# Kernel tuning notes

Measured on AMD Instinct MI355X. Metric: run time of the kernel, lower is better.

The kernel has to match this reference:

```python
import jax, jax.numpy as jnp
import numpy as np
from jax import lax

FPLANE = 64
T = 8          # num_segments
HEADS = 4
EPS = 1e-5


def _conv2d(x, w, b):
    # x: [N,C,H,W], w: [O,I,kh,kw]
    y = lax.conv_general_dilated(x, w, (1, 1), 'SAME',
                                 dimension_numbers=('NCHW', 'OIHW', 'NCHW'))
    return y + b[None, :, None, None]


def _conv3d_grouped(x, w, b, groups):
    # x: [N,C,D,H,W], w: [O, C//groups, kd,kh,kw]
    y = lax.conv_general_dilated(x, w, (1, 1, 1), 'SAME',
                                 dimension_numbers=('NCDHW', 'OIDHW', 'NCDHW'),
                                 feature_group_count=groups)
    return y + b[None, :, None, None, None]


def setup_inputs() -> dict:
    key = jax.random.key(0)
    ks = jax.random.split(key, 5)
    N, C, H, W = T * 16, FPLANE, 56, 56
    x = jax.random.normal(ks[0], (N, C, H, W), dtype=jnp.float32)
    attn_w = jax.random.normal(ks[1], (HEADS, C, 3, 3), dtype=jnp.float32) * 0.05
    attn_b = jax.random.normal(ks[2], (HEADS,), dtype=jnp.float32) * 0.05
    bn_gamma = jnp.ones((C,), dtype=jnp.float32)
    bn_beta = jnp.zeros((C,), dtype=jnp.float32)
    conv3d_w = jax.random.normal(ks[3], (2, C // 2, 3, 3, 3), dtype=jnp.float32) * 0.05
    conv3d_b = jax.random.normal(ks[4], (2,), dtype=jnp.float32) * 0.05
    return {'x': x, 'attn_w': attn_w, 'attn_b': attn_b,
            'bn_gamma': bn_gamma, 'bn_beta': bn_beta,
            'conv3d_w': conv3d_w, 'conv3d_b': conv3d_b}


def reference(x, attn_w, attn_b, bn_gamma, bn_beta, conv3d_w, conv3d_b):
    N, C, H, W = x.shape
    B = N // T
    half = C // 2
    quarter = C // 4

    # spatial attention: conv2d -> ReLU -> Sigmoid, per-head gating
    attn = jax.nn.sigmoid(jax.nn.relu(_conv2d(x, attn_w, attn_b)))  # [N,HEADS,H,W]
    xh = x.reshape(N, HEADS, C // HEADS, H, W) * attn[:, :, None]
    x2 = xh.reshape(N, C, H, W)

    # [B*T,C,H,W] -> [B,C,T,H,W]
    x5 = x2.reshape(B, T, C, H, W).transpose(0, 2, 1, 3, 4)

    # BatchNorm3d (training-mode batch statistics) + ReLU
    mean = jnp.mean(x5, axis=(0, 2, 3, 4), keepdims=True)
    var = jnp.var(x5, axis=(0, 2, 3, 4), keepdims=True)
    x_bn = (x5 - mean) * lax.rsqrt(var + EPS)
    x_bn = x_bn * bn_gamma[None, :, None, None, None] + bn_beta[None, :, None, None, None]
    x_bn_relu = jax.nn.relu(x_bn)

    # grouped conv3d gate (2 groups, 1 output channel each), tanh
    gate = jnp.tanh(_conv3d_grouped(x_bn_relu, conv3d_w, conv3d_b, groups=2))  # [B,2,T,H,W]
    g1 = gate[:, 0:1]
    g2 = gate[:, 1:2]

    x_g1 = x5[:, :half]
    x_g2 = x5[:, half:]
    y1 = g1 * x_g1
    y2 = g2 * x_g2
    r1 = x_g1 - y1
    r2 = x_g2 - y2

    pad_t = ((0, 0), (0, 0), (0, 1), (0, 0), (0, 0))
    pad_b = ((0, 0), (0, 0), (1, 0), (0, 0), (0, 0))
    y1 = jnp.pad(y1[:, :, 1:], pad_t) + r1   # left shift in time, zero pad
    y2 = jnp.pad(y2[:, :, :-1], pad_b) + r2  # right shift in time, zero pad

    # interleave sub-halves: view [B,2,C/4,T,H,W] -> permute -> [B,C/2,T,H,W]
    def interleave(y):
        return (y.reshape(B, 2, quarter, T, H, W)
                 .transpose(0, 2, 1, 3, 4, 5)
                 .reshape(B, half, T, H, W))

    y = jnp.concatenate([interleave(y1), interleave(y2)], axis=1)  # [B,C,T,H,W]
    return y.transpose(0, 2, 1, 3, 4).reshape(N, C, H, W)
```

## Files before the change

kernel.cpp:

```cpp
#include <hip/hip_runtime.h>
#include <hip/hip_bf16.h>

#define HW 3136
#define CTOT 64
#define NTOT 128
#define BB 16
#define TTT 8

static __device__ __forceinline__ float bf2f(unsigned short u) {
    union { unsigned int ui; float f; } v;
    v.ui = ((unsigned int)u) << 16;
    return v.f;
}
static __device__ __forceinline__ unsigned short f2bf(float f) {
    union { float f; unsigned int u; } v;
    v.f = f;
    unsigned int u = v.u;
    unsigned int r = (u + 0x7fffu + ((u >> 16) & 1u)) >> 16;
    return (unsigned short)r;
}

__global__ void k_repack(const float* __restrict__ aw, float* __restrict__ wpk) {
    const int idx = blockIdx.x * 256 + threadIdx.x;
    if (idx >= 2304) return;
    const int hd = idx & 3;
    const int kw = (idx >> 2) % 3;
    const int dh = (idx / 12) % 3;
    const int c = idx / 36;
    wpk[idx] = aw[hd * 576 + c * 9 + dh * 3 + kw];
}

__global__ __launch_bounds__(128) void k_attn(const float* __restrict__ x,
                                              const float* __restrict__ wpk,
                                              const float* __restrict__ ab,
                                              float* __restrict__ attn,
                                              float* __restrict__ stats) {
    const int tile = blockIdx.x % 49;
    const int n = blockIdx.x / 49;
    const int chunk = threadIdx.x >> 4;
    const int qi = threadIdx.x & 15;
    const int quad = tile * 16 + qi;
    const int q = quad % 14;
    const int h = quad / 14;
    const int w0 = q * 4;

    __shared__ float wl[2304];
    __shared__ float l[8][16][17];
    __shared__ float4 abuf[4][16];

    const float* xn = x + (size_t)n * CTOT * HW;
    const int c0 = chunk * 8;

    auto loadrows = [&](int c, float r[3][6]) {
#pragma unroll
        for (int dh = 0; dh < 3; ++dh) {
            const int hh = h + dh - 1;
            const bool v = (hh >= 0) && (hh < 56);
            const float* row = xn + c * HW + (v ? hh : h) * 56 + w0;
            const float m = v ? 1.f : 0.f;
            const float4 mid = *(const float4*)row;
            const float e0 = row[(q > 0) ? -1 : 0] * ((q > 0) ? m : 0.f);
            const float e5 = row[(q < 13) ? 4 : 3] * ((q < 13) ? m : 0.f);
            r[dh][0] = e0;
            r[dh][1] = mid.x * m; r[dh][2] = mid.y * m;
            r[dh][3] = mid.z * m; r[dh][4] = mid.w * m;
            r[dh][5] = e5;
        }
    };

    float bufA[3][6], bufB[3][6];
    loadrows(c0, bufA);

#pragma unroll
    for (int i = 0; i < 18; ++i) wl[threadIdx.x + i * 128] = wpk[threadIdx.x + i * 128];
    __syncthreads();

    float acc[4][4];
#pragma unroll
    for (int hd = 0; hd < 4; ++hd)
#pragma unroll
        for (int j = 0; j < 4; ++j) acc[hd][j] = 0.f;

    float midst[8][4];

#pragma unroll
    for (int i = 0; i < 8; ++i) {
        float (*cur)[6] = (i & 1) ? bufB : bufA;
        float (*nxt)[6] = (i & 1) ? bufA : bufB;
        if (i < 7) loadrows(c0 + i + 1, nxt);

        midst[i][0] = cur[1][1]; midst[i][1] = cur[1][2];
        midst[i][2] = cur[1][3]; midst[i][3] = cur[1][4];

        const int c = c0 + i;
#pragma unroll
        for (int dh = 0; dh < 3; ++dh) {
            const float* wb = &wl[c * 36 + dh * 12];
            const float4 wk0 = *(const float4*)(wb);
            const float4 wk1 = *(const float4*)(wb + 4);
            const float4 wk2 = *(const float4*)(wb + 8);
#pragma unroll
            for (int j = 0; j < 4; ++j) {
                const float a0 = cur[dh][j], a1 = cur[dh][j + 1], a2 = cur[dh][j + 2];
                acc[0][j] = fmaf(a0, wk0.x, fmaf(a1, wk1.x, fmaf(a2, wk2.x, acc[0][j])));
                acc[1][j] = fmaf(a0, wk0.y, fmaf(a1, wk1.y, fmaf(a2, wk2.y, acc[1][j])));
                acc[2][j] = fmaf(a0, wk0.z, fmaf(a1, wk1.z, fmaf(a2, wk2.z, acc[2][j])));
                acc[3][j] = fmaf(a0, wk0.w, fmaf(a1, wk1.w, fmaf(a2, wk2.w, acc[3][j])));
            }
        }
    }

    float* mine = &l[chunk][qi][0];
#pragma unroll
    for (int hd = 0; hd < 4; ++hd)
#pragma unroll
        for (int j = 0; j < 4; ++j) mine[hd * 4 + j] = acc[hd][j];
    __syncthreads();

    if (threadIdx.x < 64) {
        const int hd = threadIdx.x >> 4;
        const int rq = threadIdx.x & 15;
        float s0 = ab[hd], s1 = s0, s2 = s0, s3 = s0;
#pragma unroll
        for (int cch = 0; cch < 8; ++cch) {
            const float* p = &l[cch][rq][hd * 4];
            s0 += p[0]; s1 += p[1]; s2 += p[2]; s3 += p[3];
        }
        float4 o;
        o.x = s0 > 0.f ? 1.f / (1.f + __expf(-s0)) : 0.5f;
        o.y = s1 > 0.f ? 1.f / (1.f + __expf(-s1)) : 0.5f;
        o.z = s2 > 0.f ? 1.f / (1.f + __expf(-s2)) : 0.5f;
        o.w = s3 > 0.f ? 1.f / (1.f + __expf(-s3)) : 0.5f;
        *(float4*)(attn + (size_t)(n * 4 + hd) * HW + (tile * 16 + rq) * 4) = o;
        abuf[hd][rq] = o;
    }
    __syncthreads();

    const int head = chunk >> 1;
    const float4 a4 = abuf[head][qi];
    float s[8], sq[8];
#pragma unroll
    for (int i = 0; i < 8; ++i) {
        const float v0 = midst[i][0] * a4.x;
        const float v1 = midst[i][1] * a4.y;
        const float v2 = midst[i][2] * a4.z;
        const float v3 = midst[i][3] * a4.w;
        s[i] = v0 + v1 + v2 + v3;
        sq[i] = v0 * v0 + v1 * v1 + v2 * v2 + v3 * v3;
    }
#pragma unroll
    for (int i = 0; i < 8; ++i) { mine[i] = s[i]; mine[8 + i] = sq[i]; }
    __syncthreads();
    {
        const int ch2 = threadIdx.x >> 4;
        const int k = threadIdx.x & 15;
        float t = 0.f;
#pragma unroll
        for (int qq = 0; qq < 16; ++qq) t += l[ch2][qq][k];
        const int cc = ch2 * 8 + (k & 7);
        const int rep = blockIdx.x & 15;
        atomicAdd(&stats[rep * 128 + (k >> 3) * 64 + cc], t);
    }
}

__global__ void k_finalize(const float* __restrict__ stats,
                           const float* __restrict__ gamma,
                           const float* __restrict__ beta,
                           float* __restrict__ ss) {
    const int c = threadIdx.x;
    float S = 0.f, Q = 0.f;
#pragma unroll
    for (int r = 0; r < 16; ++r) {
        S += stats[r * 128 + c];
        Q += stats[r * 128 + 64 + c];
    }
    const float cnt = 401408.0f;
    const float mean = S / cnt;
    const float var = Q / cnt - mean * mean;
    const float scale = gamma[c] * rsqrtf(var + 1e-5f);
    ss[c] = scale;
    ss[64 + c] = beta[c] - mean * scale;
}

__global__ __launch_bounds__(256) void k_xbnr(const float* __restrict__ x,
                                              const float* __restrict__ attn,
                                              const float* __restrict__ ss,
                                              unsigned short* __restrict__ xbnr) {
    const int i4 = blockIdx.x * 256 + threadIdx.x;
    const int base = i4 * 4;
    const int plane = base / HW;
    const int i = base - plane * HW;
    const int c = plane & 63;
    const int n = plane >> 6;
    const float4 xv = *(const float4*)(x + (size_t)base);
    const float4 av = *(const float4*)(attn + (size_t)(n * 4 + (c >> 4)) * HW + i);
    const float sc = ss[c], sh = ss[64 + c];
    ushort4 o;
    o.x = f2bf(fmaxf(fmaf(xv.x * av.x, sc, sh), 0.f));
    o.y = f2bf(fmaxf(fmaf(xv.y * av.y, sc, sh), 0.f));
    o.z = f2bf(fmaxf(fmaf(xv.z * av.z, sc, sh), 0.f));
    o.w = f2bf(fmaxf(fmaf(xv.w * av.w, sc, sh), 0.f));
    *(ushort4*)(xbnr + (size_t)base) = o;
}

__global__ __launch_bounds__(128) void k_conv3d(const unsigned short* __restrict__ xbnr,
                                                const float* __restrict__ w3,
                                                const float* __restrict__ b3,
                                                float* __restrict__ gate) {
    const int tile = blockIdx.x % 49;
    const int oc = (blockIdx.x / 49) & 1;
    const int b = blockIdx.x / 98;
    const int chunk = threadIdx.x >> 4;
    const int qi = threadIdx.x & 15;
    const int quad = tile * 16 + qi;
    const int q = quad % 14;
    const int h = quad / 14;
    const int w0 = q * 4;

    float acc[8][4];
#pragma unroll
    for (int t = 0; t < 8; ++t)
#pragma unroll
        for (int j = 0; j < 4; ++j) acc[t][j] = 0.f;

    const int ic0 = chunk * 4;
    for (int ic = ic0; ic < ic0 + 4; ++ic) {
        const int c = oc * 32 + ic;
        const unsigned short* cbase = xbnr + (size_t)(b * 8 * 64 + c) * HW;
        const float* wic = w3 + (oc * 32 + ic) * 27;
#pragma unroll
        for (int tt = 0; tt < 8; ++tt) {
            const unsigned short* plane = cbase + (size_t)tt * (64 * HW);
#pragma unroll
            for (int dh = 0; dh < 3; ++dh) {
                const int hh = h + dh - 1;
                if (hh < 0 || hh >= 56) continue;
                const unsigned short* row = plane + hh * 56 + w0;
                const ushort4 mid = *(const ushort4*)row;
                const float f0 = (q > 0) ? bf2f(row[-1]) : 0.f;
                const float f1 = bf2f(mid.x), f2 = bf2f(mid.y);
                const float f3 = bf2f(mid.z), f4 = bf2f(mid.w);
                const float f5 = (q < 13) ? bf2f(row[4]) : 0.f;
#pragma unroll
                for (int dt = 0; dt < 3; ++dt) {
                    const int t = tt + 1 - dt;
                    if (t < 0 || t > 7) continue;
                    const float* wp = wic + dt * 9 + dh * 3;
                    const float wa = wp[0], wb = wp[1], wc = wp[2];
                    acc[t][0] = fmaf(f0, wa, fmaf(f1, wb, fmaf(f2, wc, acc[t][0])));
                    acc[t][1] = fmaf(f1, wa, fmaf(f2, wb, fmaf(f3, wc, acc[t][1])));
                    acc[t][2] = fmaf(f2, wa, fmaf(f3, wb, fmaf(f4, wc, acc[t][2])));
                    acc[t][3] = fmaf(f3, wa, fmaf(f4, wb, fmaf(f5, wc, acc[t][3])));
                }
            }
        }
    }

    __shared__ float4 l4[8 * 16 * 9];
    float4* mine = &l4[(chunk * 16 + qi) * 9];
#pragma unroll
    for (int t = 0; t < 8; ++t) {
        float4 v;
        v.x = acc[t][0]; v.y = acc[t][1]; v.z = acc[t][2]; v.w = acc[t][3];
        mine[t] = v;
    }
    __syncthreads();

    const int rt = threadIdx.x >> 4;
    const int rq = threadIdx.x & 15;
    float4 s = l4[(0 * 16 + rq) * 9 + rt];
#pragma unroll
    for (int c = 1; c < 8; ++c) {
        const float4 v = l4[(c * 16 + rq) * 9 + rt];
        s.x += v.x; s.y += v.y; s.z += v.z; s.w += v.w;
    }
    const float bb = b3[oc];
    float4 o;
    o.x = tanhf(s.x + bb);
    o.y = tanhf(s.y + bb);
    o.z = tanhf(s.z + bb);
    o.w = tanhf(s.w + bb);
    const int outquad = tile * 16 + rq;
    *(float4*)(gate + (size_t)((b * 2 + oc) * 8 + rt) * HW + outquad * 4) = o;
}

__global__ __launch_bounds__(256) void k_final(const float* __restrict__ x,
                                               const float* __restrict__ attn,
                                               const float* __restrict__ gate,
                                               float* __restrict__ out) {
    const int gt = blockIdx.x * 256 + threadIdx.x;
    const int q = gt % 14;
    int r = gt / 14;
    const int h = r % 56;
    r /= 56;
    const int co = r & 63;
    const int b = r >> 6;
    const int sp = h * 56 + q * 4;

    int cs, grp;
    if (co < 32) {
        cs = ((co & 1) << 4) | (co >> 1);
        grp = 0;
    } else {
        const int cc = co - 32;
        cs = 32 + (((cc & 1) << 4) | (cc >> 1));
        grp = 1;
    }
    const int head = cs >> 4;

    float4 x2[8], g[8];
#pragma unroll
    for (int t = 0; t < 8; ++t) {
        const int n = b * 8 + t;
        const float4 xv = *(const float4*)(x + (size_t)(n * 64 + cs) * HW + sp);
        const float4 av = *(const float4*)(attn + (size_t)(n * 4 + head) * HW + sp);
        const float4 gv = *(const float4*)(gate + (size_t)((b * 2 + grp) * 8 + t) * HW + sp);
        x2[t].x = xv.x * av.x;
        x2[t].y = xv.y * av.y;
        x2[t].z = xv.z * av.z;
        x2[t].w = xv.w * av.w;
        g[t] = gv;
    }
#pragma unroll
    for (int t = 0; t < 8; ++t) {
        float4 o;
        o.x = x2[t].x * (1.f - g[t].x);
        o.y = x2[t].y * (1.f - g[t].y);
        o.z = x2[t].z * (1.f - g[t].z);
        o.w = x2[t].w * (1.f - g[t].w);
        if (grp == 0) {
            if (t < 7) {
                o.x += x2[t + 1].x * g[t + 1].x;
                o.y += x2[t + 1].y * g[t + 1].y;
                o.z += x2[t + 1].z * g[t + 1].z;
                o.w += x2[t + 1].w * g[t + 1].w;
            }
        } else {
            if (t > 0) {
                o.x += x2[t - 1].x * g[t - 1].x;
                o.y += x2[t - 1].y * g[t - 1].y;
                o.z += x2[t - 1].z * g[t - 1].z;
                o.w += x2[t - 1].w * g[t - 1].w;
            }
        }
        *(float4*)(out + (size_t)((b * 8 + t) * 64 + co) * HW + sp) = o;
    }
}

extern "C" void kernel_launch(void* const* d_in, const int* in_sizes, int n_in,
                              void* d_out, int out_size, void* d_ws, size_t ws_size,
                              hipStream_t stream) {
    const float* x = (const float*)d_in[0];
    const float* aw = (const float*)d_in[1];
    const float* ab = (const float*)d_in[2];
    const float* gamma = (const float*)d_in[3];
    const float* beta = (const float*)d_in[4];
    const float* w3 = (const float*)d_in[5];
    const float* b3 = (const float*)d_in[6];
    float* out = (float*)d_out;

    char* ws = (char*)d_ws;
    unsigned short* xbnr = (unsigned short*)ws;
    float* attn = (float*)(ws + 51380224);
    float* gate = (float*)(ws + 57802752);
    float* stats = (float*)(ws + 57802752);
    float* ss = (float*)(ws + 61014528);
    float* wpk = (float*)(ws + 61015040);

    hipMemsetAsync(stats, 0, 8192, stream);
    k_repack<<<9, 256, 0, stream>>>(aw, wpk);
    k_attn<<<6272, 128, 0, stream>>>(x, wpk, ab, attn, stats);
    k_finalize<<<1, 64, 0, stream>>>(stats, gamma, beta, ss);
    k_xbnr<<<25088, 256, 0, stream>>>(x, attn, ss, xbnr);
    k_conv3d<<<1568, 128, 0, stream>>>(xbnr, w3, b3, gate);
    k_final<<<3136, 256, 0, stream>>>(x, attn, gate, out);
}
```

Measured before the change: 372.8 us.

## Fold weight repack into attn kernel, restructure xbnr with LDS attn, stage conv3d weights

Drops the separate repack launch; k_attn now reads the raw attention weights and permutes them into shared memory itself. k_xbnr switches to 1024 blocks, each handling one sample and one spatial slice; it stages that slice's attention values and the scale/shift table in LDS, then loops over all channels. k_conv3d first copies its output channel's 3D weights into LDS instead of reading them from global memory inside the inner loop. The aims are one fewer launch, fewer redundant attention reads, and cheaper weight access, at the cost of fewer xbnr blocks and extra sync.

```diff
diff --git a/kernel.cpp b/kernel.cpp
--- a/kernel.cpp
+++ b/kernel.cpp
@@ -20,18 +20,8 @@
     return (unsigned short)r;
 }
 
-__global__ void k_repack(const float* __restrict__ aw, float* __restrict__ wpk) {
-    const int idx = blockIdx.x * 256 + threadIdx.x;
-    if (idx >= 2304) return;
-    const int hd = idx & 3;
-    const int kw = (idx >> 2) % 3;
-    const int dh = (idx / 12) % 3;
-    const int c = idx / 36;
-    wpk[idx] = aw[hd * 576 + c * 9 + dh * 3 + kw];
-}
-
 __global__ __launch_bounds__(128) void k_attn(const float* __restrict__ x,
-                                              const float* __restrict__ wpk,
+                                              const float* __restrict__ aw,
                                               const float* __restrict__ ab,
                                               float* __restrict__ attn,
                                               float* __restrict__ stats) {
@@ -72,7 +62,14 @@
     loadrows(c0, bufA);
 
 #pragma unroll
-    for (int i = 0; i < 18; ++i) wl[threadIdx.x + i * 128] = wpk[threadIdx.x + i * 128];
+    for (int i = 0; i < 18; ++i) {
+        const int idx = threadIdx.x + i * 128;
+        const int hd = idx & 3;
+        const int kw = (idx >> 2) % 3;
+        const int dh = (idx / 12) % 3;
+        const int c = idx / 36;
+        wl[idx] = aw[hd * 576 + c * 9 + dh * 3 + kw];
+    }
     __syncthreads();
 
     float acc[4][4];
@@ -186,21 +183,34 @@
                                               const float* __restrict__ attn,
                                               const float* __restrict__ ss,
                                               unsigned short* __restrict__ xbnr) {
-    const int i4 = blockIdx.x * 256 + threadIdx.x;
-    const int base = i4 * 4;
-    const int plane = base / HW;
-    const int i = base - plane * HW;
-    const int c = plane & 63;
-    const int n = plane >> 6;
-    const float4 xv = *(const float4*)(x + (size_t)base);
-    const float4 av = *(const float4*)(attn + (size_t)(n * 4 + (c >> 4)) * HW + i);
-    const float sc = ss[c], sh = ss[64 + c];
-    ushort4 o;
-    o.x = f2bf(fmaxf(fmaf(xv.x * av.x, sc, sh), 0.f));
-    o.y = f2bf(fmaxf(fmaf(xv.y * av.y, sc, sh), 0.f));
-    o.z = f2bf(fmaxf(fmaf(xv.z * av.z, sc, sh), 0.f));
-    o.w = f2bf(fmaxf(fmaf(xv.w * av.w, sc, sh), 0.f));
-    *(ushort4*)(xbnr + (size_t)base) = o;
+    const int s = blockIdx.x & 7;
+    const int n = blockIdx.x >> 3;
+    const int base_sp = s * 392;
+
+    __shared__ float al[4 * 392];
+    __shared__ float ssl[128];
+    for (int i = threadIdx.x; i < 392; i += 256) {
+        const int hd = i / 98;
+        const int j = i - hd * 98;
+        ((float4*)al)[hd * 98 + j] =
+            *(const float4*)(attn + (size_t)(n * 4 + hd) * HW + base_sp + j * 4);
+    }
+    if (threadIdx.x < 128) ssl[threadIdx.x] = ss[threadIdx.x];
+    __syncthreads();
+
+    for (int wi = threadIdx.x; wi < 6272; wi += 256) {
+        const int c = wi / 98;
+        const int j = wi - c * 98;
+        const float sc = ssl[c], sh = ssl[64 + c];
+        const float4 xv = *(const float4*)(x + (size_t)(n * 64 + c) * HW + base_sp + j * 4);
+        const float4 av = ((const float4*)al)[(c >> 4) * 98 + j];
+        ushort4 o;
+        o.x = f2bf(fmaxf(fmaf(xv.x * av.x, sc, sh), 0.f));
+        o.y = f2bf(fmaxf(fmaf(xv.y * av.y, sc, sh), 0.f));
+        o.z = f2bf(fmaxf(fmaf(xv.z * av.z, sc, sh), 0.f));
+        o.w = f2bf(fmaxf(fmaf(xv.w * av.w, sc, sh), 0.f));
+        *(ushort4*)(xbnr + (size_t)(n * 64 + c) * HW + base_sp + j * 4) = o;
+    }
 }
 
 __global__ __launch_bounds__(128) void k_conv3d(const unsigned short* __restrict__ xbnr,
@@ -217,6 +227,10 @@
     const int h = quad / 14;
     const int w0 = q * 4;
 
+    __shared__ float wlds[864];
+    for (int i = threadIdx.x; i < 864; i += 128) wlds[i] = w3[oc * 864 + i];
+    __syncthreads();
+
     float acc[8][4];
 #pragma unroll
     for (int t = 0; t < 8; ++t)
@@ -227,7 +241,7 @@
     for (int ic = ic0; ic < ic0 + 4; ++ic) {
         const int c = oc * 32 + ic;
         const unsigned short* cbase = xbnr + (size_t)(b * 8 * 64 + c) * HW;
-        const float* wic = w3 + (oc * 32 + ic) * 27;
+        const float* wic = &wlds[ic * 27];
 #pragma unroll
         for (int tt = 0; tt < 8; ++tt) {
             const unsigned short* plane = cbase + (size_t)tt * (64 * HW);
@@ -365,13 +379,11 @@
     float* gate = (float*)(ws + 57802752);
     float* stats = (float*)(ws + 57802752);
     float* ss = (float*)(ws + 61014528);
-    float* wpk = (float*)(ws + 61015040);
 
     hipMemsetAsync(stats, 0, 8192, stream);
-    k_repack<<<9, 256, 0, stream>>>(aw, wpk);
-    k_attn<<<6272, 128, 0, stream>>>(x, wpk, ab, attn, stats);
+    k_attn<<<6272, 128, 0, stream>>>(x, aw, ab, attn, stats);
     k_finalize<<<1, 64, 0, stream>>>(stats, gamma, beta, ss);
-    k_xbnr<<<25088, 256, 0, stream>>>(x, attn, ss, xbnr);
+    k_xbnr<<<1024, 256, 0, stream>>>(x, attn, ss, xbnr);
     k_conv3d<<<1568, 128, 0, stream>>>(xbnr, w3, b3, gate);
     k_final<<<3136, 256, 0, stream>>>(x, attn, gate, out);
 }
```

Measured after the change: 358.6 us. 1.04x faster.
